# Kernel tuning notes

Hardware: AMD Instinct MI355X
Metric: run time of the kernel (lower is better)

Reference implementation:

```python
import jax, jax.numpy as jnp
import numpy as np

E = 1024   # embd_size
H = 16     # heads_num
DH = E // H
DFF = 4 * E
B, T = 2, 2048


def layer_norm(x, g, b, eps=1e-5):
    mu = jnp.mean(x, axis=-1, keepdims=True)
    var = jnp.var(x, axis=-1, keepdims=True)
    return (x - mu) * jax.lax.rsqrt(var + eps) * g + b


def setup_inputs() -> dict:
    key = jax.random.key(0)
    ks = jax.random.split(key, 12)
    s = 0.02
    return {
        "x": jax.random.normal(ks[0], (B, T, E), dtype=jnp.float32),
        "Wq": jax.random.normal(ks[1], (E, E), dtype=jnp.float32) * s,
        "Wk": jax.random.normal(ks[2], (E, E), dtype=jnp.float32) * s,
        "Wv": jax.random.normal(ks[3], (E, E), dtype=jnp.float32) * s,
        "Wo": jax.random.normal(ks[4], (E, E), dtype=jnp.float32) * s,
        "bo": jnp.zeros((E,), dtype=jnp.float32),
        "W1": jax.random.normal(ks[5], (E, DFF), dtype=jnp.float32) * s,
        "b1": jnp.zeros((DFF,), dtype=jnp.float32),
        "W2": jax.random.normal(ks[6], (DFF, E), dtype=jnp.float32) * s,
        "b2": jnp.zeros((E,), dtype=jnp.float32),
        "g1": jnp.ones((E,), dtype=jnp.float32),
        "be1": jnp.zeros((E,), dtype=jnp.float32),
        "g2": jnp.ones((E,), dtype=jnp.float32),
        "be2": jnp.zeros((E,), dtype=jnp.float32),
    }


def reference(x, Wq, Wk, Wv, Wo, bo, W1, b1, W2, b2, g1, be1, g2, be2):
    Bx, Tx, C = x.shape
    # --- self-attention sublayer ---
    h = layer_norm(x, g1, be1)
    # per-head projections; heads concatenated along output dim == stacked weights
    q = (h @ Wq).reshape(Bx, Tx, H, DH)  # [B,T,H,Dh]
    k = (h @ Wk).reshape(Bx, Tx, H, DH)
    v = (h @ Wv).reshape(Bx, Tx, H, DH)
    # NOTE: original scales by full embd_size**-0.5 (C = x.shape[-1]), not head_size
    scale = C ** (-0.5)
    scores = jnp.einsum("bqhd,bkhd->bhqk", q, k) * scale  # [B,H,T,T]
    mask = jnp.tril(jnp.ones((Tx, Tx), dtype=bool))
    scores = jnp.where(mask, scores, -jnp.inf)
    attn = jax.nn.softmax(scores, axis=-1)
    o = jnp.einsum("bhqk,bkhd->bqhd", attn, v).reshape(Bx, Tx, C)
    sa = o @ Wo + bo
    x = x + sa
    # --- feed-forward sublayer ---
    h2 = layer_norm(x, g2, be2)
    ff = jax.nn.relu(h2 @ W1 + b1) @ W2 + b2
    return x + ff
```

## Files before the change

### kernel.cpp

```cpp
#include <hip/hip_runtime.h>
#include <hip/hip_bf16.h>
#include <math.h>

#define Bn 2
#define Tn 2048
#define En 1024
#define Hn 16
#define DFFn 4096
#define Mn (Bn*Tn)
#define QKVLD 3072

typedef __hip_bfloat16 bf16;
typedef unsigned short u16;
typedef __attribute__((ext_vector_type(8))) short short8;
typedef __attribute__((ext_vector_type(4))) float f32x4;

typedef __attribute__((address_space(1))) const void cg_void;
typedef __attribute__((address_space(3))) void lds_void;

__device__ __forceinline__ u16 f2bf(float f) {
    bf16 h = __float2bfloat16(f);
    u16 u; __builtin_memcpy(&u, &h, 2); return u;
}

__global__ __launch_bounds__(256)
void transpose_w(const float* __restrict__ src, u16* __restrict__ dst,
                 int R, int C) {
    __shared__ float t[64][65];
    const int r0 = blockIdx.y * 64, c0 = blockIdx.x * 64;
    const int tr = threadIdx.x >> 6, tc = threadIdx.x & 63;
#pragma unroll
    for (int i = 0; i < 16; i++)
        t[tr + i * 4][tc] = src[(size_t)(r0 + tr + i * 4) * C + c0 + tc];
    __syncthreads();
#pragma unroll
    for (int i = 0; i < 16; i++)
        dst[(size_t)(c0 + tr + i * 4) * R + r0 + tc] = f2bf(t[tc][tr + i * 4]);
}

__global__ __launch_bounds__(256)
void ln_kernel(const float* __restrict__ x, const float* __restrict__ g,
               const float* __restrict__ b, u16* __restrict__ out) {
    const int row = blockIdx.x;
    const int tid = threadIdx.x;
    const float* xp = x + (size_t)row * En;
    float v[4];
    float s = 0.f, sq = 0.f;
#pragma unroll
    for (int i = 0; i < 4; i++) {
        v[i] = xp[tid + i * 256];
        s += v[i];
        sq += v[i] * v[i];
    }
    __shared__ float rs[256], rq[256];
    rs[tid] = s; rq[tid] = sq;
    __syncthreads();
    for (int st = 128; st > 0; st >>= 1) {
        if (tid < st) { rs[tid] += rs[tid + st]; rq[tid] += rq[tid + st]; }
        __syncthreads();
    }
    const float mu  = rs[0] * (1.0f / En);
    const float var = rq[0] * (1.0f / En) - mu * mu;
    const float inv = rsqrtf(var + 1e-5f);
#pragma unroll
    for (int i = 0; i < 4; i++) {
        const int c = tid + i * 256;
        out[(size_t)row * En + c] = f2bf((v[i] - mu) * inv * g[c] + b[c]);
    }
}

template<int TM, int HAS_BIAS, int RELU, int HAS_RES, int OUT_F32>
__global__ __launch_bounds__(256)
void gemm_bt(const u16* __restrict__ A, int ldA,
             const u16* __restrict__ Wt, int ldW,
             const float* __restrict__ bias, const float* __restrict__ res,
             void* __restrict__ Cout, int ldC, int Kd) {
    constexpr int IF = TM / 32;
    __shared__ __align__(16) u16 As[TM * 32];
    __shared__ __align__(16) u16 Bs[128 * 32];
    const int tid  = threadIdx.x;
    const int lane = tid & 63, wv = tid >> 6;
    const int quad = lane >> 4, l16 = lane & 15;
    const int m0 = blockIdx.y * TM, n0 = blockIdx.x * 128;
    const int rw = (wv >> 1) * (TM / 2), cw = (wv & 1) * 64;
    const int lr = lane >> 2, lc = (lane & 3) * 8;

    f32x4 acc[IF][4] = {};

    for (int kt = 0; kt < Kd; kt += 32) {
        __syncthreads();
#pragma unroll
        for (int t = 0; t < TM / 64; t++) {
            const int row = wv * (TM / 4) + t * 16;
            __builtin_amdgcn_global_load_lds(
                (cg_void*)(const void*)&A[(size_t)(m0 + row + lr) * ldA + kt + lc],
                (lds_void*)(void*)&As[row * 32], 16, 0, 0);
        }
#pragma unroll
        for (int t = 0; t < 2; t++) {
            const int row = wv * 32 + t * 16;
            __builtin_amdgcn_global_load_lds(
                (cg_void*)(const void*)&Wt[(size_t)(n0 + row + lr) * ldW + kt + lc],
                (lds_void*)(void*)&Bs[row * 32], 16, 0, 0);
        }
        __syncthreads();

        short8 af[IF], bfr[4];
#pragma unroll
        for (int i = 0; i < IF; i++)
            af[i] = *(const short8*)&As[(rw + i * 16 + l16) * 32 + quad * 8];
#pragma unroll
        for (int j = 0; j < 4; j++)
            bfr[j] = *(const short8*)&Bs[(cw + j * 16 + l16) * 32 + quad * 8];
#pragma unroll
        for (int i = 0; i < IF; i++)
#pragma unroll
            for (int j = 0; j < 4; j++)
                acc[i][j] = __builtin_amdgcn_mfma_f32_16x16x32_bf16(
                    af[i], bfr[j], acc[i][j], 0, 0, 0);
    }

#pragma unroll
    for (int i = 0; i < IF; i++) {
#pragma unroll
        for (int r = 0; r < 4; r++) {
            const int gm = m0 + rw + i * 16 + quad * 4 + r;
#pragma unroll
            for (int j = 0; j < 4; j++) {
                const int gn = n0 + cw + j * 16 + l16;
                float c = acc[i][j][r];
                if (HAS_BIAS) c += bias[gn];
                if (RELU) c = fmaxf(c, 0.f);
                if (HAS_RES) c += res[(size_t)gm * ldC + gn];
                if (OUT_F32) ((float*)Cout)[(size_t)gm * ldC + gn] = c;
                else         ((u16*)Cout)[(size_t)gm * ldC + gn] = f2bf(c);
            }
        }
    }
}

__global__ __launch_bounds__(256)
void flash_attn(u16* __restrict__ QKV) {
    const int hh = blockIdx.y, bb = blockIdx.z;
    const int tid  = threadIdx.x;
    const int lane = tid & 63, wv = tid >> 6;
    const int quad = lane >> 4, l16 = lane & 15;

    __shared__ __align__(16) u16 Qs[64 * 80];
    __shared__ __align__(16) u16 Ks[64 * 80];
    __shared__ __align__(16) u16 Vt[64 * 80];
    __shared__ __align__(16) u16 Ps[4][16 * 70];

    const size_t rowbase = (size_t)(bb * Tn) * QKVLD;
    const int sr = tid >> 2, scg = tid & 3;
    const int vkey = tid & 63, vw = tid >> 6;
    const float SC = 0.03125f * 1.44269504089f;

    for (int qsel = 0; qsel < 2; qsel++) {
        const int qt = qsel ? (31 - blockIdx.x) : blockIdx.x;

        __syncthreads();
        {
            const size_t qb = rowbase + (size_t)(qt * 64 + sr) * QKVLD + hh * 64;
            *(uint4*)&Qs[sr * 80 + scg * 8]       = *(const uint4*)&QKV[qb + scg * 8];
            *(uint4*)&Qs[sr * 80 + (scg + 4) * 8] = *(const uint4*)&QKV[qb + (scg + 4) * 8];
        }
        uint4 kreg0, kreg1, vreg0, vreg1;
        {
            const size_t kb = rowbase + (size_t)(sr) * QKVLD + 1024 + hh * 64;
            kreg0 = *(const uint4*)&QKV[kb + scg * 8];
            kreg1 = *(const uint4*)&QKV[kb + (scg + 4) * 8];
            const size_t vb = rowbase + (size_t)(vkey) * QKVLD + 2048 + hh * 64 + vw * 16;
            vreg0 = *(const uint4*)&QKV[vb];
            vreg1 = *(const uint4*)&QKV[vb + 8];
        }
        __syncthreads();
        short8 qf[2];
        qf[0] = *(const short8*)&Qs[(wv * 16 + l16) * 80 + quad * 8];
        qf[1] = *(const short8*)&Qs[(wv * 16 + l16) * 80 + 32 + quad * 8];

        f32x4 ot[4] = {};
        float m2 = -INFINITY, lrow = 0.f;

        for (int kt = 0; kt <= qt; kt++) {
            __syncthreads();
            {
                *(uint4*)&Ks[sr * 80 + scg * 8]       = kreg0;
                *(uint4*)&Ks[sr * 80 + (scg + 4) * 8] = kreg1;
                u16 vtmp[16];
                *(uint4*)&vtmp[0] = vreg0;
                *(uint4*)&vtmp[8] = vreg1;
#pragma unroll
                for (int u = 0; u < 16; u++)
                    Vt[(vw * 16 + u) * 80 + vkey] = vtmp[u];
            }
            if (kt < qt) {
                const size_t kb = rowbase + (size_t)((kt + 1) * 64 + sr) * QKVLD + 1024 + hh * 64;
                kreg0 = *(const uint4*)&QKV[kb + scg * 8];
                kreg1 = *(const uint4*)&QKV[kb + (scg + 4) * 8];
                const size_t vb = rowbase + (size_t)((kt + 1) * 64 + vkey) * QKVLD + 2048 + hh * 64 + vw * 16;
                vreg0 = *(const uint4*)&QKV[vb];
                vreg1 = *(const uint4*)&QKV[vb + 8];
            }
            __syncthreads();

            f32x4 st[4] = {};
#pragma unroll
            for (int ks = 0; ks < 2; ks++)
#pragma unroll
                for (int i = 0; i < 4; i++) {
                    short8 kf = *(const short8*)&Ks[(i * 16 + l16) * 80 + ks * 32 + quad * 8];
                    st[i] = __builtin_amdgcn_mfma_f32_16x16x32_bf16(kf, qf[ks], st[i], 0, 0, 0);
                }

            float p[4][4];
            float tmax = -INFINITY;
            if (kt == qt) {
                const int qloc = wv * 16 + l16;
#pragma unroll
                for (int i = 0; i < 4; i++)
#pragma unroll
                    for (int r = 0; r < 4; r++) {
                        float s = st[i][r] * SC;
                        if (i * 16 + quad * 4 + r > qloc) s = -INFINITY;
                        p[i][r] = s;
                        tmax = fmaxf(tmax, s);
                    }
            } else {
#pragma unroll
                for (int i = 0; i < 4; i++)
#pragma unroll
                    for (int r = 0; r < 4; r++) {
                        const float s = st[i][r] * SC;
                        p[i][r] = s;
                        tmax = fmaxf(tmax, s);
                    }
            }
            tmax = fmaxf(tmax, __shfl_xor(tmax, 16));
            tmax = fmaxf(tmax, __shfl_xor(tmax, 32));

            const float mnew = fmaxf(m2, tmax);
            const float alpha = exp2f(m2 - mnew);
            m2 = mnew;
            float psum = 0.f;
#pragma unroll
            for (int i = 0; i < 4; i++)
#pragma unroll
                for (int r = 0; r < 4; r++) {
                    const float e = exp2f(p[i][r] - mnew);
                    p[i][r] = e;
                    psum += e;
                }
            psum += __shfl_xor(psum, 16);
            psum += __shfl_xor(psum, 32);
            lrow = lrow * alpha + psum;
#pragma unroll
            for (int i = 0; i < 4; i++) ot[i] *= alpha;

#pragma unroll
            for (int i = 0; i < 4; i++)
#pragma unroll
                for (int r = 0; r < 4; r++)
                    Ps[wv][l16 * 70 + i * 16 + quad * 4 + r] = f2bf(p[i][r]);
            asm volatile("s_waitcnt lgkmcnt(0)" ::: "memory");

#pragma unroll
            for (int ks = 0; ks < 2; ks++) {
                short8 pf = *(const short8*)&Ps[wv][l16 * 70 + ks * 32 + quad * 8];
#pragma unroll
                for (int i = 0; i < 4; i++) {
                    short8 vf = *(const short8*)&Vt[(i * 16 + l16) * 80 + ks * 32 + quad * 8];
                    ot[i] = __builtin_amdgcn_mfma_f32_16x16x32_bf16(vf, pf, ot[i], 0, 0, 0);
                }
            }
        }

        const float linv = 1.0f / lrow;
        const size_t obase = rowbase + (size_t)(qt * 64 + wv * 16 + l16) * QKVLD + hh * 64;
#pragma unroll
        for (int i = 0; i < 4; i++)
#pragma unroll
            for (int r = 0; r < 4; r++)
                QKV[obase + i * 16 + quad * 4 + r] = f2bf(ot[i][r] * linv);
    }
}

extern "C" void kernel_launch(void* const* d_in, const int* in_sizes, int n_in,
                              void* d_out, int out_size, void* d_ws, size_t ws_size,
                              hipStream_t stream) {
    const float* x   = (const float*)d_in[0];
    const float* Wq  = (const float*)d_in[1];
    const float* Wk  = (const float*)d_in[2];
    const float* Wv  = (const float*)d_in[3];
    const float* Wo  = (const float*)d_in[4];
    const float* bo  = (const float*)d_in[5];
    const float* W1  = (const float*)d_in[6];
    const float* b1  = (const float*)d_in[7];
    const float* W2  = (const float*)d_in[8];
    const float* b2  = (const float*)d_in[9];
    const float* g1  = (const float*)d_in[10];
    const float* be1 = (const float*)d_in[11];
    const float* g2  = (const float*)d_in[12];
    const float* be2 = (const float*)d_in[13];

    char* wsb = (char*)d_ws;
    u16*   QKV = (u16*)wsb;
    u16*   F1  = (u16*)wsb;
    u16*   W2T = (u16*)(wsb + 16u * 1024 * 1024);
    float* X1  = (float*)(wsb + 24u * 1024 * 1024);
    u16*   h     = (u16*)d_out;
    u16*   WT    = (u16*)((char*)d_out + 8u * 1024 * 1024);
    u16*   WqkvT = WT;
    u16*   WoT   = WT + 3u * 1024 * 1024;
    u16*   W1T   = WT;

    transpose_w<<<dim3(16, 16), 256, 0, stream>>>(Wq, WqkvT,                 1024, 1024);
    transpose_w<<<dim3(16, 16), 256, 0, stream>>>(Wk, WqkvT + 1024u * 1024,  1024, 1024);
    transpose_w<<<dim3(16, 16), 256, 0, stream>>>(Wv, WqkvT + 2048u * 1024,  1024, 1024);
    transpose_w<<<dim3(16, 16), 256, 0, stream>>>(Wo, WoT,                   1024, 1024);

    ln_kernel<<<Mn, 256, 0, stream>>>(x, g1, be1, h);

    gemm_bt<128, 0, 0, 0, 0><<<dim3(24, 32), 256, 0, stream>>>(
        h, En, WqkvT, En, nullptr, nullptr, QKV, QKVLD, En);

    flash_attn<<<dim3(16, Hn, Bn), 256, 0, stream>>>(QKV);

    gemm_bt<64, 1, 0, 1, 1><<<dim3(8, 64), 256, 0, stream>>>(
        QKV, QKVLD, WoT, En, bo, x, X1, En, En);

    transpose_w<<<dim3(64, 16), 256, 0, stream>>>(W1, W1T, 1024, 4096);
    transpose_w<<<dim3(16, 64), 256, 0, stream>>>(W2, W2T, 4096, 1024);

    ln_kernel<<<Mn, 256, 0, stream>>>(X1, g2, be2, h);

    gemm_bt<128, 1, 1, 0, 0><<<dim3(16, 32), 256, 0, stream>>>(
        h, En, W1T, En, b1, nullptr, F1, 2048, En);
    gemm_bt<64, 0, 0, 1, 1><<<dim3(8, 64), 256, 0, stream>>>(
        F1, 2048, W2T, DFFn, nullptr, X1, X1, En, 2048);
    gemm_bt<128, 1, 1, 0, 0><<<dim3(16, 32), 256, 0, stream>>>(
        h, En, W1T + 2048u * 1024, En, b1 + 2048, nullptr, F1, 2048, En);
    gemm_bt<64, 1, 0, 1, 1><<<dim3(8, 64), 256, 0, stream>>>(
        F1, 2048, W2T + 2048, DFFn, b2, X1, (float*)d_out, En, 2048);
}
```

Measured before the change: 406.6 us.

## Double-buffer attention K/V tiles, swizzle GEMM LDS, merge weight transposes

The flash attention kernel now double-buffers its K and V tiles in LDS. The next tile is written after the current tile's compute, so each iteration needs one barrier instead of two. Row padding changes from 80 to 88 and the output is written with ushort4 vector stores. The GEMM applies an XOR swizzle to the LDS column chunk so fragment reads avoid bank conflicts, and the four 1024x1024 weight transposes are merged into one launch. These target barrier stalls, LDS bank conflicts and launch overhead, at the cost of more LDS per block, which may lower occupancy.

```diff
diff --git a/kernel.cpp b/kernel.cpp
--- a/kernel.cpp
+++ b/kernel.cpp
@@ -18,9 +18,32 @@
 typedef __attribute__((address_space(1))) const void cg_void;
 typedef __attribute__((address_space(3))) void lds_void;
 
+#define HBAR() asm volatile("s_waitcnt lgkmcnt(0)\n\ts_barrier" ::: "memory")
+
 __device__ __forceinline__ u16 f2bf(float f) {
     bf16 h = __float2bfloat16(f);
     u16 u; __builtin_memcpy(&u, &h, 2); return u;
+}
+
+__global__ __launch_bounds__(256)
+void transpose_w4(const float* __restrict__ s0, const float* __restrict__ s1,
+                  const float* __restrict__ s2, const float* __restrict__ s3,
+                  u16* __restrict__ d0, u16* __restrict__ d1,
+                  u16* __restrict__ d2, u16* __restrict__ d3) {
+    const float* src = (blockIdx.z == 0) ? s0 : (blockIdx.z == 1) ? s1
+                     : (blockIdx.z == 2) ? s2 : s3;
+    u16* dst = (blockIdx.z == 0) ? d0 : (blockIdx.z == 1) ? d1
+             : (blockIdx.z == 2) ? d2 : d3;
+    __shared__ float t[64][65];
+    const int r0 = blockIdx.y * 64, c0 = blockIdx.x * 64;
+    const int tr = threadIdx.x >> 6, tc = threadIdx.x & 63;
+#pragma unroll
+    for (int i = 0; i < 16; i++)
+        t[tr + i * 4][tc] = src[(size_t)(r0 + tr + i * 4) * 1024 + c0 + tc];
+    __syncthreads();
+#pragma unroll
+    for (int i = 0; i < 16; i++)
+        dst[(size_t)(c0 + tr + i * 4) * 1024 + r0 + tc] = f2bf(t[tc][tr + i * 4]);
 }
 
 __global__ __launch_bounds__(256)
@@ -83,7 +106,9 @@
     const int quad = lane >> 4, l16 = lane & 15;
     const int m0 = blockIdx.y * TM, n0 = blockIdx.x * 128;
     const int rw = (wv >> 1) * (TM / 2), cw = (wv & 1) * 64;
-    const int lr = lane >> 2, lc = (lane & 3) * 8;
+    const int lr  = lane >> 2;
+    const int gsw = ((lane & 3) ^ ((lane >> 3) & 3)) * 8;
+    const int psw = (quad ^ ((l16 >> 1) & 3)) * 8;
 
     f32x4 acc[IF][4] = {};
 
@@ -93,14 +118,14 @@
         for (int t = 0; t < TM / 64; t++) {
             const int row = wv * (TM / 4) + t * 16;
             __builtin_amdgcn_global_load_lds(
-                (cg_void*)(const void*)&A[(size_t)(m0 + row + lr) * ldA + kt + lc],
+                (cg_void*)(const void*)&A[(size_t)(m0 + row + lr) * ldA + kt + gsw],
                 (lds_void*)(void*)&As[row * 32], 16, 0, 0);
         }
 #pragma unroll
         for (int t = 0; t < 2; t++) {
             const int row = wv * 32 + t * 16;
             __builtin_amdgcn_global_load_lds(
-                (cg_void*)(const void*)&Wt[(size_t)(n0 + row + lr) * ldW + kt + lc],
+                (cg_void*)(const void*)&Wt[(size_t)(n0 + row + lr) * ldW + kt + gsw],
                 (lds_void*)(void*)&Bs[row * 32], 16, 0, 0);
         }
         __syncthreads();
@@ -108,10 +133,10 @@
         short8 af[IF], bfr[4];
 #pragma unroll
         for (int i = 0; i < IF; i++)
-            af[i] = *(const short8*)&As[(rw + i * 16 + l16) * 32 + quad * 8];
+            af[i] = *(const short8*)&As[(rw + i * 16 + l16) * 32 + psw];
 #pragma unroll
         for (int j = 0; j < 4; j++)
-            bfr[j] = *(const short8*)&Bs[(cw + j * 16 + l16) * 32 + quad * 8];
+            bfr[j] = *(const short8*)&Bs[(cw + j * 16 + l16) * 32 + psw];
 #pragma unroll
         for (int i = 0; i < IF; i++)
 #pragma unroll
@@ -146,9 +171,9 @@
     const int lane = tid & 63, wv = tid >> 6;
     const int quad = lane >> 4, l16 = lane & 15;
 
-    __shared__ __align__(16) u16 Qs[64 * 80];
-    __shared__ __align__(16) u16 Ks[64 * 80];
-    __shared__ __align__(16) u16 Vt[64 * 80];
+    __shared__ __align__(16) u16 Qs[64 * 88];
+    __shared__ __align__(16) u16 Ks[2][64 * 88];
+    __shared__ __align__(16) u16 Vt[2][64 * 88];
     __shared__ __align__(16) u16 Ps[4][16 * 70];
 
     const size_t rowbase = (size_t)(bb * Tn) * QKVLD;
@@ -159,57 +184,54 @@
     for (int qsel = 0; qsel < 2; qsel++) {
         const int qt = qsel ? (31 - blockIdx.x) : blockIdx.x;
 
-        __syncthreads();
+        HBAR();
         {
             const size_t qb = rowbase + (size_t)(qt * 64 + sr) * QKVLD + hh * 64;
-            *(uint4*)&Qs[sr * 80 + scg * 8]       = *(const uint4*)&QKV[qb + scg * 8];
-            *(uint4*)&Qs[sr * 80 + (scg + 4) * 8] = *(const uint4*)&QKV[qb + (scg + 4) * 8];
+            *(uint4*)&Qs[sr * 88 + scg * 8]       = *(const uint4*)&QKV[qb + scg * 8];
+            *(uint4*)&Qs[sr * 88 + (scg + 4) * 8] = *(const uint4*)&QKV[qb + (scg + 4) * 8];
         }
         uint4 kreg0, kreg1, vreg0, vreg1;
         {
-            const size_t kb = rowbase + (size_t)(sr) * QKVLD + 1024 + hh * 64;
+            const size_t kb = rowbase + (size_t)sr * QKVLD + 1024 + hh * 64;
             kreg0 = *(const uint4*)&QKV[kb + scg * 8];
             kreg1 = *(const uint4*)&QKV[kb + (scg + 4) * 8];
-            const size_t vb = rowbase + (size_t)(vkey) * QKVLD + 2048 + hh * 64 + vw * 16;
+            const size_t vb = rowbase + (size_t)vkey * QKVLD + 2048 + hh * 64 + vw * 16;
             vreg0 = *(const uint4*)&QKV[vb];
             vreg1 = *(const uint4*)&QKV[vb + 8];
-        }
-        __syncthreads();
+            *(uint4*)&Ks[0][sr * 88 + scg * 8]       = kreg0;
+            *(uint4*)&Ks[0][sr * 88 + (scg + 4) * 8] = kreg1;
+            u16 vtmp[16];
+            *(uint4*)&vtmp[0] = vreg0;
+            *(uint4*)&vtmp[8] = vreg1;
+#pragma unroll
+            for (int u = 0; u < 16; u++)
+                Vt[0][(vw * 16 + u) * 88 + vkey] = vtmp[u];
+        }
+        if (qt >= 1) {
+            const size_t kb = rowbase + (size_t)(64 + sr) * QKVLD + 1024 + hh * 64;
+            kreg0 = *(const uint4*)&QKV[kb + scg * 8];
+            kreg1 = *(const uint4*)&QKV[kb + (scg + 4) * 8];
+            const size_t vb = rowbase + (size_t)(64 + vkey) * QKVLD + 2048 + hh * 64 + vw * 16;
+            vreg0 = *(const uint4*)&QKV[vb];
+            vreg1 = *(const uint4*)&QKV[vb + 8];
+        }
+        HBAR();
         short8 qf[2];
-        qf[0] = *(const short8*)&Qs[(wv * 16 + l16) * 80 + quad * 8];
-        qf[1] = *(const short8*)&Qs[(wv * 16 + l16) * 80 + 32 + quad * 8];
+        qf[0] = *(const short8*)&Qs[(wv * 16 + l16) * 88 + quad * 8];
+        qf[1] = *(const short8*)&Qs[(wv * 16 + l16) * 88 + 32 + quad * 8];
 
         f32x4 ot[4] = {};
         float m2 = -INFINITY, lrow = 0.f;
 
         for (int kt = 0; kt <= qt; kt++) {
-            __syncthreads();
-            {
-                *(uint4*)&Ks[sr * 80 + scg * 8]       = kreg0;
-                *(uint4*)&Ks[sr * 80 + (scg + 4) * 8] = kreg1;
-                u16 vtmp[16];
-                *(uint4*)&vtmp[0] = vreg0;
-                *(uint4*)&vtmp[8] = vreg1;
-#pragma unroll
-                for (int u = 0; u < 16; u++)
-                    Vt[(vw * 16 + u) * 80 + vkey] = vtmp[u];
-            }
-            if (kt < qt) {
-                const size_t kb = rowbase + (size_t)((kt + 1) * 64 + sr) * QKVLD + 1024 + hh * 64;
-                kreg0 = *(const uint4*)&QKV[kb + scg * 8];
-                kreg1 = *(const uint4*)&QKV[kb + (scg + 4) * 8];
-                const size_t vb = rowbase + (size_t)((kt + 1) * 64 + vkey) * QKVLD + 2048 + hh * 64 + vw * 16;
-                vreg0 = *(const uint4*)&QKV[vb];
-                vreg1 = *(const uint4*)&QKV[vb + 8];
-            }
-            __syncthreads();
+            const int cur = kt & 1;
 
             f32x4 st[4] = {};
 #pragma unroll
             for (int ks = 0; ks < 2; ks++)
 #pragma unroll
                 for (int i = 0; i < 4; i++) {
-                    short8 kf = *(const short8*)&Ks[(i * 16 + l16) * 80 + ks * 32 + quad * 8];
+                    short8 kf = *(const short8*)&Ks[cur][(i * 16 + l16) * 88 + ks * 32 + quad * 8];
                     st[i] = __builtin_amdgcn_mfma_f32_16x16x32_bf16(kf, qf[ks], st[i], 0, 0, 0);
                 }
 
@@ -269,19 +291,43 @@
                 short8 pf = *(const short8*)&Ps[wv][l16 * 70 + ks * 32 + quad * 8];
 #pragma unroll
                 for (int i = 0; i < 4; i++) {
-                    short8 vf = *(const short8*)&Vt[(i * 16 + l16) * 80 + ks * 32 + quad * 8];
+                    short8 vf = *(const short8*)&Vt[cur][(i * 16 + l16) * 88 + ks * 32 + quad * 8];
                     ot[i] = __builtin_amdgcn_mfma_f32_16x16x32_bf16(vf, pf, ot[i], 0, 0, 0);
                 }
             }
+
+            if (kt < qt) {
+                *(uint4*)&Ks[cur ^ 1][sr * 88 + scg * 8]       = kreg0;
+                *(uint4*)&Ks[cur ^ 1][sr * 88 + (scg + 4) * 8] = kreg1;
+                u16 vtmp[16];
+                *(uint4*)&vtmp[0] = vreg0;
+                *(uint4*)&vtmp[8] = vreg1;
+#pragma unroll
+                for (int u = 0; u < 16; u++)
+                    Vt[cur ^ 1][(vw * 16 + u) * 88 + vkey] = vtmp[u];
+                if (kt + 1 < qt) {
+                    const size_t kb = rowbase + (size_t)((kt + 2) * 64 + sr) * QKVLD + 1024 + hh * 64;
+                    kreg0 = *(const uint4*)&QKV[kb + scg * 8];
+                    kreg1 = *(const uint4*)&QKV[kb + (scg + 4) * 8];
+                    const size_t vb = rowbase + (size_t)((kt + 2) * 64 + vkey) * QKVLD + 2048 + hh * 64 + vw * 16;
+                    vreg0 = *(const uint4*)&QKV[vb];
+                    vreg1 = *(const uint4*)&QKV[vb + 8];
+                }
+                HBAR();
+            }
         }
 
         const float linv = 1.0f / lrow;
         const size_t obase = rowbase + (size_t)(qt * 64 + wv * 16 + l16) * QKVLD + hh * 64;
 #pragma unroll
-        for (int i = 0; i < 4; i++)
-#pragma unroll
-            for (int r = 0; r < 4; r++)
-                QKV[obase + i * 16 + quad * 4 + r] = f2bf(ot[i][r] * linv);
+        for (int i = 0; i < 4; i++) {
+            ushort4 o4;
+            o4.x = f2bf(ot[i][0] * linv);
+            o4.y = f2bf(ot[i][1] * linv);
+            o4.z = f2bf(ot[i][2] * linv);
+            o4.w = f2bf(ot[i][3] * linv);
+            *(ushort4*)&QKV[obase + i * 16 + quad * 4] = o4;
+        }
     }
 }
 
@@ -314,10 +360,9 @@
     u16*   WoT   = WT + 3u * 1024 * 1024;
     u16*   W1T   = WT;
 
-    transpose_w<<<dim3(16, 16), 256, 0, stream>>>(Wq, WqkvT,                 1024, 1024);
-    transpose_w<<<dim3(16, 16), 256, 0, stream>>>(Wk, WqkvT + 1024u * 1024,  1024, 1024);
-    transpose_w<<<dim3(16, 16), 256, 0, stream>>>(Wv, WqkvT + 2048u * 1024,  1024, 1024);
-    transpose_w<<<dim3(16, 16), 256, 0, stream>>>(Wo, WoT,                   1024, 1024);
+    transpose_w4<<<dim3(16, 16, 4), 256, 0, stream>>>(
+        Wq, Wk, Wv, Wo,
+        WqkvT, WqkvT + 1024u * 1024, WqkvT + 2048u * 1024, WoT);
 
     ln_kernel<<<Mn, 256, 0, stream>>>(x, g1, be1, h);
 
```

New measurement: 393.9 us. 1.03x faster.
